# Optimization experiments

Measured on AMD Instinct MI355X. Metric: run time of the kernel, lower is better.

## Reference

```python
import jax, jax.numpy as jnp
import numpy as np

N = 50000   # nodes
E = 640000  # edges
IN = 256    # in_dim
H = 128     # hidden
OUT = 40    # out_dim
EPS = 1e-5  # BatchNorm eps


def setup_inputs() -> dict:
    key = jax.random.key(0)
    ks = jax.random.split(key, 14)
    x = jax.random.normal(ks[0], (N, IN), jnp.float32)
    edge_index = jax.random.randint(ks[1], (2, E), 0, N)
    def lin(k, fan_in, shape):
        return jax.random.normal(k, shape, jnp.float32) / np.float32(np.sqrt(fan_in))
    return {
        "x": x,
        "edge_index": edge_index,
        # block 0 (256 -> 128, has res_proj)
        "W0": lin(ks[2], IN, (IN, H)),
        "b0": jnp.zeros((H,), jnp.float32),
        "g0": jnp.ones((H,), jnp.float32),
        "be0": jnp.zeros((H,), jnp.float32),
        "pW": lin(ks[3], IN, (IN, H)),
        "pb": jnp.zeros((H,), jnp.float32),
        # block 1 (128 -> 128, identity residual)
        "W1": lin(ks[4], H, (H, H)),
        "b1": jnp.zeros((H,), jnp.float32),
        "g1": jnp.ones((H,), jnp.float32),
        "be1": jnp.zeros((H,), jnp.float32),
        # head
        "hW": lin(ks[5], H, (H, OUT)),
        "hb": jnp.zeros((OUT,), jnp.float32),
    }


def _gcn_conv(x, W, b, edge_index):
    """GCNConv(improved=True): x' = D^-1/2 (A + 2I) D^-1/2 (x W) + b."""
    h = x @ W  # [N, dout]
    row, col = edge_index[0], edge_index[1]  # source -> target
    # degree of A + 2I (edge_weight = 1, self-loop fill = 2.0)
    deg = jnp.zeros((N,), h.dtype).at[col].add(1.0) + 2.0
    dis = jax.lax.rsqrt(deg)  # deg > 0 always (self-loops)
    norm = dis[row] * dis[col]  # [E]
    # neighbor aggregation: scatter-add normalized messages to targets
    agg = jnp.zeros_like(h).at[col].add(norm[:, None] * h[row])
    # self-loop contribution with weight 2.0
    agg = agg + (2.0 * dis * dis)[:, None] * h
    return agg + b


def _bn(x, gamma, beta):
    # batch statistics (training-mode BatchNorm math), biased variance
    m = jnp.mean(x, axis=0)
    v = jnp.mean(jnp.square(x - m), axis=0)
    return (x - m) * jax.lax.rsqrt(v + EPS) * gamma + beta


def reference(x, edge_index, W0, b0, g0, be0, pW, pb, W1, b1, g1, be1, hW, hb):
    # block 0: conv -> bn -> relu -> (+ res_proj(x))
    out = jax.nn.relu(_bn(_gcn_conv(x, W0, b0, edge_index), g0, be0))
    x1 = out + (x @ pW + pb)
    # block 1: conv -> bn -> relu -> (+ identity)
    out = jax.nn.relu(_bn(_gcn_conv(x1, W1, b1, edge_index), g1, be1))
    x2 = out + x1
    return x2 @ hW + hb  # [N, OUT]
```

## Files before the change

kernel.cpp:

```cpp
#include <hip/hip_runtime.h>

#define H 128
#define IN_DIM 256
#define OUT_DIM 40
#define EPS 1e-5f

typedef unsigned short ushortT;
typedef __attribute__((ext_vector_type(8))) short bf16x8;
typedef __attribute__((ext_vector_type(4))) float f32x4;

static __device__ __forceinline__ ushortT f2bf(float f) {
    union { float f; unsigned u; } v; v.f = f;
    unsigned r = v.u + 0x7FFF + ((v.u >> 16) & 1);
    return (ushortT)(r >> 16);
}
static __device__ __forceinline__ unsigned pk2(float a, float b) {
    return (unsigned)f2bf(a) | ((unsigned)f2bf(b) << 16);
}
static __device__ __forceinline__ float bflo(unsigned v) {
    union { unsigned u; float f; } t; t.u = v << 16; return t.f;
}
static __device__ __forceinline__ float bfhi(unsigned v) {
    union { unsigned u; float f; } t; t.u = v & 0xFFFF0000u; return t.f;
}
static __device__ __forceinline__ float i2f(int v) {
    union { int i; float f; } t; t.i = v; return t.f;
}
static __device__ __forceinline__ int f2i(float v) {
    union { float f; int i; } t; t.f = v; return t.i;
}


__global__ __launch_bounds__(256) void count_xcd(const int* __restrict__ ei, int E, int nper,
                                                 int* __restrict__ cnt) {
    int xcd = blockIdx.x & 7;
    int nchunk = gridDim.x >> 3;
    int chunk = blockIdx.x >> 3;
    int csz = (E + nchunk - 1) / nchunk;
    int beg = chunk * csz;
    int end = min(E, beg + csz);
    for (int e = beg + (int)threadIdx.x; e < end; e += 256) {
        int c = ei[E + e];
        if (c / nper == xcd) atomicAdd(&cnt[c], 1);
    }
}

__global__ __launch_bounds__(256) void scan_block_sum(const int* __restrict__ cnt, int* __restrict__ bsum,
                                                      float* __restrict__ dis, int N) {
    __shared__ int s[256];
    int i = blockIdx.x * 256 + threadIdx.x;
    int c = (i < N) ? cnt[i] : -1;
    int v = (i < N) ? c + 1 : 0;
    if (i < N) dis[i] = rsqrtf((float)c + 2.0f);
    s[threadIdx.x] = v;
    __syncthreads();
    for (int o = 128; o > 0; o >>= 1) {
        if (threadIdx.x < o) s[threadIdx.x] += s[threadIdx.x + o];
        __syncthreads();
    }
    if (threadIdx.x == 0) bsum[blockIdx.x] = s[0];
}

__global__ void scan_tops(const int* __restrict__ bsum, int* __restrict__ boff, int* __restrict__ rowptrN, int nb) {
    __shared__ int s[256];
    int t = threadIdx.x;
    int v = (t < nb) ? bsum[t] : 0;
    s[t] = v;
    __syncthreads();
    for (int o = 1; o < 256; o <<= 1) {
        int u = (t >= o) ? s[t - o] : 0;
        __syncthreads();
        s[t] += u;
        __syncthreads();
    }
    if (t < nb) boff[t] = s[t] - v;
    if (t == 255) *rowptrN = s[255];
}

__global__ __launch_bounds__(256) void scan_final(const int* __restrict__ cnt, const int* __restrict__ boff,
                                                  const float* __restrict__ dis,
                                                  int* __restrict__ rowptr, int* __restrict__ cursor,
                                                  int2* __restrict__ recs, int N) {
    __shared__ int s[256];
    int t = threadIdx.x;
    int i = blockIdx.x * 256 + t;
    int v = (i < N) ? cnt[i] + 1 : 0;
    s[t] = v;
    __syncthreads();
    for (int o = 1; o < 256; o <<= 1) {
        int u = (t >= o) ? s[t - o] : 0;
        __syncthreads();
        s[t] += u;
        __syncthreads();
    }
    if (i < N) {
        int e = boff[blockIdx.x] + s[t] - v;
        rowptr[i] = e;
        cursor[i] = e + 1;
        float d = dis[i];
        int2 r; r.x = i; r.y = f2i(2.0f * d * d);
        recs[e] = r;
    }
}

__global__ __launch_bounds__(256) void fill_xcd(const int* __restrict__ ei, int E, int nper,
                                                const float* __restrict__ dis,
                                                int* __restrict__ cursor, int2* __restrict__ recs) {
    int xcd = blockIdx.x & 7;
    int nchunk = gridDim.x >> 3;
    int chunk = blockIdx.x >> 3;
    int csz = (E + nchunk - 1) / nchunk;
    int beg = chunk * csz;
    int end = min(E, beg + csz);
    for (int e = beg + (int)threadIdx.x; e < end; e += 256) {
        int c = ei[E + e];
        if (c / nper == xcd) {
            int r = ei[e];
            int slot = atomicAdd(&cursor[c], 1);
            int2 rec; rec.x = r; rec.y = f2i(dis[r] * dis[c]);
            recs[slot] = rec;
        }
    }
}


__global__ __launch_bounds__(256) void prep_weights(const float* __restrict__ W0, const float* __restrict__ pW,
                                                    const float* __restrict__ W1, const float* __restrict__ hW,
                                                    ushortT* __restrict__ Wt0, ushortT* __restrict__ WtP,
                                                    ushortT* __restrict__ Wt1, ushortT* __restrict__ WtH,
                                                    int* __restrict__ cnt, float* __restrict__ stats, int N) {
    int i = blockIdx.x * 256 + threadIdx.x;
    if (i < 32768) { int n = i >> 8, k = i & 255; Wt0[i] = f2bf(W0[k * 128 + n]); WtP[i] = f2bf(pW[k * 128 + n]); }
    if (i < 16384) { int n = i >> 7, k = i & 127; Wt1[i] = f2bf(W1[k * 128 + n]); }
    if (i < 6144)  { int n = i >> 7, k = i & 127; WtH[i] = (n < OUT_DIM) ? f2bf(hW[k * OUT_DIM + n]) : (ushortT)0; }
    if (i < N) cnt[i] = 0;
    if (i < 512) stats[i] = 0.f;
}


static __device__ __forceinline__ void g0_loads(const float* __restrict__ X, int brow, int kc,
                                                int tid, int N, float4 pf[4]) {
#pragma unroll
    for (int i = 0; i < 4; ++i) {
        int idx = i * 512 + tid;
        int row = idx >> 5, c4 = idx & 31;
        int gr = brow + row;
        pf[i] = make_float4(0.f, 0.f, 0.f, 0.f);
        if (gr < N) pf[i] = *(const float4*)&X[(size_t)gr * IN_DIM + kc * 128 + c4 * 4];
    }
}
static __device__ __forceinline__ void g0_write(ushortT* __restrict__ Sbuf, int tid, const float4 pf[4]) {
#pragma unroll
    for (int i = 0; i < 4; ++i) {
        int idx = i * 512 + tid;
        int row = idx >> 5, c4 = idx & 31;
        uint2 p;
        p.x = pk2(pf[i].x, pf[i].y);
        p.y = pk2(pf[i].z, pf[i].w);
        *(uint2*)&Sbuf[row * 136 + c4 * 4] = p;
    }
}

__global__ __launch_bounds__(512) void mgemm0p(const float* __restrict__ X,
                                               const ushortT* __restrict__ Wt0,
                                               const ushortT* __restrict__ WtP,
                                               const float* __restrict__ pb,
                                               ushortT* __restrict__ Oh,
                                               ushortT* __restrict__ Op,
                                               int N, int ntiles) {
    __shared__ __align__(16) ushortT S[2][64 * 136];
    int tid = threadIdx.x;
    int w = tid >> 6, lane = tid & 63;
    int lm = lane & 15, lk = lane >> 4;
    int mat = w >> 2;
    int colbase = (w & 3) * 32;
    const ushortT* Wt = mat ? WtP : Wt0;

    bf16x8 breg[2][8];
#pragma unroll
    for (int nt = 0; nt < 2; ++nt)
#pragma unroll
        for (int kk = 0; kk < 8; ++kk)
            breg[nt][kk] = *(const bf16x8*)&Wt[(size_t)(colbase + nt * 16 + lm) * IN_DIM + kk * 32 + lk * 8];
    float bb[2];
    bb[0] = mat ? pb[colbase + lm] : 0.f;
    bb[1] = mat ? pb[colbase + 16 + lm] : 0.f;
    ushortT* O = mat ? Op : Oh;

    int bid = blockIdx.x, G = gridDim.x;
    int T = (ntiles - 1 - bid) / G + 1;
    int U = 2 * T;

    float4 pf[4];
    g0_loads(X, bid * 64, 0, tid, N, pf);
    g0_write(S[0], tid, pf);

    f32x4 acc[4][2];
#pragma unroll
    for (int mt = 0; mt < 4; ++mt)
#pragma unroll
        for (int nt = 0; nt < 2; ++nt) acc[mt][nt] = (f32x4)0.f;

    for (int u = 0; u < U; ++u) {
        __syncthreads();
        if (u + 1 < U) {
            int t1 = bid + ((u + 1) >> 1) * G;
            g0_loads(X, t1 * 64, (u + 1) & 1, tid, N, pf);
        }
        int kc = u & 1;
        const ushortT* Sc = S[u & 1];
#pragma unroll
        for (int kk = 0; kk < 4; ++kk) {
            bf16x8 af[4];
#pragma unroll
            for (int mt = 0; mt < 4; ++mt)
                af[mt] = *(const bf16x8*)&Sc[(mt * 16 + lm) * 136 + kk * 32 + lk * 8];
#pragma unroll
            for (int nt = 0; nt < 2; ++nt)
#pragma unroll
                for (int mt = 0; mt < 4; ++mt)
                    acc[mt][nt] = __builtin_amdgcn_mfma_f32_16x16x32_bf16(af[mt], breg[nt][kc * 4 + kk], acc[mt][nt], 0, 0, 0);
        }
        if (u + 1 < U) g0_write(S[(u + 1) & 1], tid, pf);
        if (kc == 1) {
            int t = bid + (u >> 1) * G;
            int brow = t * 64;
#pragma unroll
            for (int mt = 0; mt < 4; ++mt)
#pragma unroll
                for (int nt = 0; nt < 2; ++nt) {
                    int col = colbase + nt * 16 + lm;
#pragma unroll
                    for (int j = 0; j < 4; ++j) {
                        int r = brow + mt * 16 + lk * 4 + j;
                        if (r < N) O[(size_t)r * 128 + col] = f2bf(acc[mt][nt][j] + bb[nt]);
                    }
                    acc[mt][nt] = (f32x4)0.f;
                }
        }
    }
}


__global__ __launch_bounds__(512) void mgemm1_fused(const uint4* __restrict__ aggb,
                                                    const uint4* __restrict__ projb,
                                                    const float* __restrict__ stats,
                                                    const float* __restrict__ g,
                                                    const float* __restrict__ be,
                                                    const ushortT* __restrict__ Wt1,
                                                    ushortT* __restrict__ O,
                                                    uint4* __restrict__ x1b,
                                                    int N) {
    __shared__ __align__(16) ushortT S[17408];
    __shared__ float sc[128], sh[128];
    int tid = threadIdx.x;
    int brow = blockIdx.x * 128;

    if (tid < 128) {
        float mean = stats[tid] / (float)N;
        float var = stats[128 + tid] / (float)N - mean * mean;
        float inv = rsqrtf(var + EPS);
        float s = g[tid] * inv;
        sc[tid] = s;
        sh[tid] = be[tid] - mean * s;
    }
    __syncthreads();

#pragma unroll
    for (int i = 0; i < 4; ++i) {
        int idx = i * 512 + tid;
        int row = idx >> 4, q = idx & 15;
        int gr = brow + row;
        uint4 a = make_uint4(0u, 0u, 0u, 0u), p = a;
        if (gr < N) {
            size_t gidx = (size_t)gr * 16 + q;
            a = aggb[gidx];
            p = projb[gidx];
        }
        int ch = q * 8;
        float v0 = fmaxf(fmaf(bflo(a.x), sc[ch + 0], sh[ch + 0]), 0.f) + bflo(p.x);
        float v1 = fmaxf(fmaf(bfhi(a.x), sc[ch + 1], sh[ch + 1]), 0.f) + bfhi(p.x);
        float v2 = fmaxf(fmaf(bflo(a.y), sc[ch + 2], sh[ch + 2]), 0.f) + bflo(p.y);
        float v3 = fmaxf(fmaf(bfhi(a.y), sc[ch + 3], sh[ch + 3]), 0.f) + bfhi(p.y);
        float v4 = fmaxf(fmaf(bflo(a.z), sc[ch + 4], sh[ch + 4]), 0.f) + bflo(p.z);
        float v5 = fmaxf(fmaf(bfhi(a.z), sc[ch + 5], sh[ch + 5]), 0.f) + bfhi(p.z);
        float v6 = fmaxf(fmaf(bflo(a.w), sc[ch + 6], sh[ch + 6]), 0.f) + bflo(p.w);
        float v7 = fmaxf(fmaf(bfhi(a.w), sc[ch + 7], sh[ch + 7]), 0.f) + bfhi(p.w);
        uint4 pv;
        pv.x = pk2(v0, v1);
        pv.y = pk2(v2, v3);
        pv.z = pk2(v4, v5);
        pv.w = pk2(v6, v7);
        *(uint4*)&S[row * 136 + q * 8] = pv;
        if (gr < N) x1b[(size_t)gr * 16 + q] = pv;
    }
    __syncthreads();

    int w = tid >> 6, lane = tid & 63;
    int lm = lane & 15, lk = lane >> 4;
    int rh = (w >> 2) * 64;
    int colbase = (w & 3) * 32;

    bf16x8 breg[2][4];
#pragma unroll
    for (int nt = 0; nt < 2; ++nt)
#pragma unroll
        for (int ks = 0; ks < 4; ++ks)
            breg[nt][ks] = *(const bf16x8*)&Wt1[(size_t)(colbase + nt * 16 + lm) * H + ks * 32 + lk * 8];

    f32x4 acc[4][2];
#pragma unroll
    for (int mt = 0; mt < 4; ++mt)
#pragma unroll
        for (int nt = 0; nt < 2; ++nt) acc[mt][nt] = (f32x4)0.f;

#pragma unroll
    for (int ks = 0; ks < 4; ++ks) {
        bf16x8 af[4];
#pragma unroll
        for (int mt = 0; mt < 4; ++mt)
            af[mt] = *(const bf16x8*)&S[(rh + mt * 16 + lm) * 136 + ks * 32 + lk * 8];
#pragma unroll
        for (int nt = 0; nt < 2; ++nt)
#pragma unroll
            for (int mt = 0; mt < 4; ++mt)
                acc[mt][nt] = __builtin_amdgcn_mfma_f32_16x16x32_bf16(af[mt], breg[nt][ks], acc[mt][nt], 0, 0, 0);
    }

    __syncthreads();
#pragma unroll
    for (int mt = 0; mt < 4; ++mt)
#pragma unroll
        for (int nt = 0; nt < 2; ++nt) {
            int col = colbase + nt * 16 + lm;
#pragma unroll
            for (int j = 0; j < 4; ++j) {
                int row = rh + mt * 16 + lk * 4 + j;
                S[row * 136 + col] = f2bf(acc[mt][nt][j]);
            }
        }
    __syncthreads();
#pragma unroll
    for (int i = 0; i < 4; ++i) {
        int idx = i * 512 + tid;
        int row = idx >> 4, colq = idx & 15;
        int gr = brow + row;
        if (gr < N) {
            uint4 v = *(const uint4*)&S[row * 136 + colq * 8];
            *(uint4*)&O[(size_t)gr * 128 + colq * 8] = v;
        }
    }
}


__global__ __launch_bounds__(256) void aggregate_rec(const ushortT* __restrict__ h,
                                                     const int* __restrict__ rowptr,
                                                     const int2* __restrict__ recs,
                                                     ushortT* __restrict__ aggb, int N) {
    int n = blockIdx.x * 4 + (threadIdx.x >> 6);
    if (n >= N) return;
    int lane = threadIdx.x & 63;
    int half = lane >> 5, cl = lane & 31;
    int beg = rowptr[n], end = rowptr[n + 1];
    const uint2* h2 = (const uint2*)h;
    float a0 = 0.f, a1 = 0.f, a2 = 0.f, a3 = 0.f;
    float b0 = 0.f, b1 = 0.f, b2 = 0.f, b3 = 0.f;
    int idx = beg + half;
    for (; idx + 2 < end; idx += 4) {
        int2 r0 = recs[idx];
        int2 r1 = recs[idx + 2];
        uint2 v0 = h2[(size_t)r0.x * 32 + cl];
        uint2 v1 = h2[(size_t)r1.x * 32 + cl];
        float n0 = i2f(r0.y), n1 = i2f(r1.y);
        a0 = fmaf(n0, bflo(v0.x), a0); a1 = fmaf(n0, bfhi(v0.x), a1);
        a2 = fmaf(n0, bflo(v0.y), a2); a3 = fmaf(n0, bfhi(v0.y), a3);
        b0 = fmaf(n1, bflo(v1.x), b0); b1 = fmaf(n1, bfhi(v1.x), b1);
        b2 = fmaf(n1, bflo(v1.y), b2); b3 = fmaf(n1, bfhi(v1.y), b3);
    }
    if (idx < end) {
        int2 r0 = recs[idx];
        uint2 v0 = h2[(size_t)r0.x * 32 + cl];
        float n0 = i2f(r0.y);
        a0 = fmaf(n0, bflo(v0.x), a0); a1 = fmaf(n0, bfhi(v0.x), a1);
        a2 = fmaf(n0, bflo(v0.y), a2); a3 = fmaf(n0, bfhi(v0.y), a3);
    }
    a0 += b0; a1 += b1; a2 += b2; a3 += b3;
    a0 += __shfl_xor(a0, 32);
    a1 += __shfl_xor(a1, 32);
    a2 += __shfl_xor(a2, 32);
    a3 += __shfl_xor(a3, 32);
    if (half == 0) {
        uint2 o;
        o.x = pk2(a0, a1);
        o.y = pk2(a2, a3);
        ((uint2*)aggb)[(size_t)n * 32 + cl] = o;
    }
}


__global__ __launch_bounds__(256) void stats_bf(const unsigned* __restrict__ v, int totalU,
                                                float* __restrict__ sums) {
    int tid = blockIdx.x * 256 + threadIdx.x;
    int stride = gridDim.x * 256;
    float sx = 0.f, sy = 0.f, qx = 0.f, qy = 0.f;
    for (int i = tid; i < totalU; i += stride) {
        unsigned u = v[i];
        float a = bflo(u), b = bfhi(u);
        sx += a; sy += b;
        qx = fmaf(a, a, qx); qy = fmaf(b, b, qy);
    }
    __shared__ float l0[256], l1[256], l2[256], l3[256];
    int t = threadIdx.x;
    l0[t] = sx; l1[t] = sy; l2[t] = qx; l3[t] = qy;
    __syncthreads();
    if (t < 64) {
        sx = (l0[t] + l0[t + 64]) + (l0[t + 128] + l0[t + 192]);
        sy = (l1[t] + l1[t + 64]) + (l1[t + 128] + l1[t + 192]);
        qx = (l2[t] + l2[t + 64]) + (l2[t + 128] + l2[t + 192]);
        qy = (l3[t] + l3[t + 64]) + (l3[t + 128] + l3[t + 192]);
        atomicAdd(&sums[2 * t], sx);
        atomicAdd(&sums[2 * t + 1], sy);
        atomicAdd(&sums[128 + 2 * t], qx);
        atomicAdd(&sums[128 + 2 * t + 1], qy);
    }
}


__global__ __launch_bounds__(256) void head_fused(const uint4* __restrict__ aggb,
                                                  const uint4* __restrict__ x1b,
                                                  const float* __restrict__ stats,
                                                  const float* __restrict__ g,
                                                  const float* __restrict__ be,
                                                  const ushortT* __restrict__ WtH,
                                                  const float* __restrict__ hb,
                                                  float* __restrict__ out, int N) {
    __shared__ __align__(16) ushortT As[64][136];
    __shared__ __align__(16) ushortT Bs[48][136];
    __shared__ float sc[128], sh[128];

    int tid = threadIdx.x;
    int brow = blockIdx.x * 64;
    int w = tid >> 6, lane = tid & 63;
    int lm = lane & 15, lk = lane >> 4;

    if (tid < 128) {
        float mean = stats[tid] / (float)N;
        float var = stats[128 + tid] / (float)N - mean * mean;
        float inv = rsqrtf(var + EPS);
        float s = g[tid] * inv;
        sc[tid] = s;
        sh[tid] = be[tid] - mean * s;
    }
    if (tid < 192) {
        int row = tid >> 2, q = tid & 3;
        const uint4* src = (const uint4*)&WtH[(size_t)row * H + q * 32];
        uint4 a = src[0], b = src[1], c = src[2], d = src[3];
        uint4* dst = (uint4*)&Bs[row][q * 32];
        dst[0] = a; dst[1] = b; dst[2] = c; dst[3] = d;
    }
    __syncthreads();
#pragma unroll
    for (int k = 0; k < 4; ++k) {
        int idx = k * 256 + tid;
        int row = idx >> 4, colq = idx & 15;
        int gr = brow + row;
        uint4 a = make_uint4(0u, 0u, 0u, 0u), x = a;
        if (gr < N) {
            size_t gidx = (size_t)brow * 16 + idx;
            a = aggb[gidx];
            x = x1b[gidx];
        }
        int ch = colq * 8;
        float v0 = fmaxf(fmaf(bflo(a.x), sc[ch + 0], sh[ch + 0]), 0.f) + bflo(x.x);
        float v1 = fmaxf(fmaf(bfhi(a.x), sc[ch + 1], sh[ch + 1]), 0.f) + bfhi(x.x);
        float v2 = fmaxf(fmaf(bflo(a.y), sc[ch + 2], sh[ch + 2]), 0.f) + bflo(x.y);
        float v3 = fmaxf(fmaf(bfhi(a.y), sc[ch + 3], sh[ch + 3]), 0.f) + bfhi(x.y);
        float v4 = fmaxf(fmaf(bflo(a.z), sc[ch + 4], sh[ch + 4]), 0.f) + bflo(x.z);
        float v5 = fmaxf(fmaf(bfhi(a.z), sc[ch + 5], sh[ch + 5]), 0.f) + bfhi(x.z);
        float v6 = fmaxf(fmaf(bflo(a.w), sc[ch + 6], sh[ch + 6]), 0.f) + bflo(x.w);
        float v7 = fmaxf(fmaf(bfhi(a.w), sc[ch + 7], sh[ch + 7]), 0.f) + bfhi(x.w);
        uint4 pv;
        pv.x = pk2(v0, v1);
        pv.y = pk2(v2, v3);
        pv.z = pk2(v4, v5);
        pv.w = pk2(v6, v7);
        *(uint4*)&As[row][colq * 8] = pv;
    }
    __syncthreads();

    f32x4 acc[3];
#pragma unroll
    for (int nt = 0; nt < 3; ++nt) acc[nt] = (f32x4)0.f;
#pragma unroll
    for (int ks = 0; ks < 4; ++ks) {
        bf16x8 a = *(const bf16x8*)&As[w * 16 + lm][ks * 32 + lk * 8];
#pragma unroll
        for (int nt = 0; nt < 3; ++nt) {
            bf16x8 b = *(const bf16x8*)&Bs[nt * 16 + lm][ks * 32 + lk * 8];
            acc[nt] = __builtin_amdgcn_mfma_f32_16x16x32_bf16(a, b, acc[nt], 0, 0, 0);
        }
    }
#pragma unroll
    for (int nt = 0; nt < 3; ++nt) {
        int col = nt * 16 + lm;
        if (col < OUT_DIM) {
            float bbv = hb[col];
#pragma unroll
            for (int j = 0; j < 4; ++j) {
                int r = brow + w * 16 + lk * 4 + j;
                if (r < N) out[(size_t)r * OUT_DIM + col] = acc[nt][j] + bbv;
            }
        }
    }
}


extern "C" void kernel_launch(void* const* d_in, const int* in_sizes, int n_in,
                              void* d_out, int out_size, void* d_ws, size_t ws_size,
                              hipStream_t stream) {
    const float* x   = (const float*)d_in[0];
    const int*   ei  = (const int*)d_in[1];
    const float* W0  = (const float*)d_in[2];
    const float* g0  = (const float*)d_in[4];
    const float* be0 = (const float*)d_in[5];
    const float* pW  = (const float*)d_in[6];
    const float* pb  = (const float*)d_in[7];
    const float* W1  = (const float*)d_in[8];
    const float* g1  = (const float*)d_in[10];
    const float* be1 = (const float*)d_in[11];
    const float* hW  = (const float*)d_in[12];
    const float* hb  = (const float*)d_in[13];
    float* out = (float*)d_out;

    int N = in_sizes[0] / IN_DIM;
    int E = in_sizes[1] / 2;
    size_t NH = (size_t)N * H;

    ushortT* hb16   = (ushortT*)d_ws;
    ushortT* aggb   = hb16 + NH;
    ushortT* projb  = aggb + NH;
    ushortT* x1b    = projb + NH;
    float*   dis    = (float*)(x1b + NH);
    int*     cnt    = (int*)(dis + N);
    int*     rowptr = cnt + N;
    int*     cursor = rowptr + (N + 1);
    int2*    recs   = (int2*)(cursor + N);
    float*   stats  = (float*)(recs + (E + N));
    ushortT* Wt0    = (ushortT*)(stats + 512);
    ushortT* WtP    = Wt0 + 128 * 256;
    ushortT* Wt1    = WtP + 128 * 256;
    ushortT* WtH    = Wt1 + 128 * 128;
    int*     bsum   = (int*)(WtH + 48 * 128);
    int*     boff   = bsum + 256;
    float*   stats0 = stats;
    float*   stats1 = stats + 256;

    int nb = (N + 255) / 256;
    int g64 = (N + 63) / 64;
    int g128 = (N + 127) / 128;
    int gAgg = (N + 3) / 4;
    int ntiles = g64;
    int gPersist = (ntiles + 1) / 2;

    prep_weights<<<196, 256, 0, stream>>>(W0, pW, W1, hW, Wt0, WtP, Wt1, WtH, cnt, stats, N);
    count_xcd<<<2048, 256, 0, stream>>>(ei, E, (N + 7) / 8, cnt);
    scan_block_sum<<<nb, 256, 0, stream>>>(cnt, bsum, dis, N);
    scan_tops<<<1, 256, 0, stream>>>(bsum, boff, &rowptr[N], nb);
    scan_final<<<nb, 256, 0, stream>>>(cnt, boff, dis, rowptr, cursor, recs, N);
    fill_xcd<<<2048, 256, 0, stream>>>(ei, E, (N + 7) / 8, dis, cursor, recs);

    mgemm0p<<<gPersist, 512, 0, stream>>>(x, Wt0, WtP, pb, hb16, projb, N, ntiles);
    aggregate_rec<<<gAgg, 256, 0, stream>>>(hb16, rowptr, recs, aggb, N);
    stats_bf<<<256, 256, 0, stream>>>((const unsigned*)aggb, (int)(NH / 2), stats0);

    mgemm1_fused<<<g128, 512, 0, stream>>>((const uint4*)aggb, (const uint4*)projb, stats0, g0, be0,
                                           Wt1, hb16, (uint4*)x1b, N);
    aggregate_rec<<<gAgg, 256, 0, stream>>>(hb16, rowptr, recs, aggb, N);
    stats_bf<<<256, 256, 0, stream>>>((const unsigned*)aggb, (int)(NH / 2), stats1);

    head_fused<<<g64, 256, 0, stream>>>((const uint4*)aggb, (const uint4*)x1b, stats1, g1, be1,
                                        WtH, hb, out, N);
}
```

Measured before the change: 261.6 us.

## Replace persistent first GEMM with one-tile-per-block kernel and staged coalesced stores

```diff
diff --git a/kernel.cpp b/kernel.cpp
--- a/kernel.cpp
+++ b/kernel.cpp
@@ -161,15 +161,16 @@
     }
 }
 
-__global__ __launch_bounds__(512) void mgemm0p(const float* __restrict__ X,
+__global__ __launch_bounds__(512) void mgemm0d(const float* __restrict__ X,
                                                const ushortT* __restrict__ Wt0,
                                                const ushortT* __restrict__ WtP,
                                                const float* __restrict__ pb,
                                                ushortT* __restrict__ Oh,
                                                ushortT* __restrict__ Op,
-                                               int N, int ntiles) {
-    __shared__ __align__(16) ushortT S[2][64 * 136];
+                                               int N) {
+    __shared__ __align__(16) ushortT S2[2][64 * 136];
     int tid = threadIdx.x;
+    int brow = blockIdx.x * 64;
     int w = tid >> 6, lane = tid & 63;
     int lm = lane & 15, lk = lane >> 4;
     int mat = w >> 2;
@@ -185,15 +186,12 @@
     float bb[2];
     bb[0] = mat ? pb[colbase + lm] : 0.f;
     bb[1] = mat ? pb[colbase + 16 + lm] : 0.f;
-    ushortT* O = mat ? Op : Oh;
-
-    int bid = blockIdx.x, G = gridDim.x;
-    int T = (ntiles - 1 - bid) / G + 1;
-    int U = 2 * T;
 
     float4 pf[4];
-    g0_loads(X, bid * 64, 0, tid, N, pf);
-    g0_write(S[0], tid, pf);
+    g0_loads(X, brow, 0, tid, N, pf);
+    g0_write(S2[0], tid, pf);
+    __syncthreads();
+    g0_loads(X, brow, 1, tid, N, pf);
 
     f32x4 acc[4][2];
 #pragma unroll
@@ -201,42 +199,56 @@
 #pragma unroll
         for (int nt = 0; nt < 2; ++nt) acc[mt][nt] = (f32x4)0.f;
 
-    for (int u = 0; u < U; ++u) {
-        __syncthreads();
-        if (u + 1 < U) {
-            int t1 = bid + ((u + 1) >> 1) * G;
-            g0_loads(X, t1 * 64, (u + 1) & 1, tid, N, pf);
-        }
-        int kc = u & 1;
-        const ushortT* Sc = S[u & 1];
-#pragma unroll
-        for (int kk = 0; kk < 4; ++kk) {
-            bf16x8 af[4];
+#pragma unroll
+    for (int kk = 0; kk < 4; ++kk) {
+        bf16x8 af[4];
+#pragma unroll
+        for (int mt = 0; mt < 4; ++mt)
+            af[mt] = *(const bf16x8*)&S2[0][(mt * 16 + lm) * 136 + kk * 32 + lk * 8];
+#pragma unroll
+        for (int nt = 0; nt < 2; ++nt)
 #pragma unroll
             for (int mt = 0; mt < 4; ++mt)
-                af[mt] = *(const bf16x8*)&Sc[(mt * 16 + lm) * 136 + kk * 32 + lk * 8];
-#pragma unroll
-            for (int nt = 0; nt < 2; ++nt)
-#pragma unroll
-                for (int mt = 0; mt < 4; ++mt)
-                    acc[mt][nt] = __builtin_amdgcn_mfma_f32_16x16x32_bf16(af[mt], breg[nt][kc * 4 + kk], acc[mt][nt], 0, 0, 0);
-        }
-        if (u + 1 < U) g0_write(S[(u + 1) & 1], tid, pf);
-        if (kc == 1) {
-            int t = bid + (u >> 1) * G;
-            int brow = t * 64;
+                acc[mt][nt] = __builtin_amdgcn_mfma_f32_16x16x32_bf16(af[mt], breg[nt][kk], acc[mt][nt], 0, 0, 0);
+    }
+    g0_write(S2[1], tid, pf);
+    __syncthreads();
+#pragma unroll
+    for (int kk = 0; kk < 4; ++kk) {
+        bf16x8 af[4];
+#pragma unroll
+        for (int mt = 0; mt < 4; ++mt)
+            af[mt] = *(const bf16x8*)&S2[1][(mt * 16 + lm) * 136 + kk * 32 + lk * 8];
+#pragma unroll
+        for (int nt = 0; nt < 2; ++nt)
 #pragma unroll
             for (int mt = 0; mt < 4; ++mt)
-#pragma unroll
-                for (int nt = 0; nt < 2; ++nt) {
-                    int col = colbase + nt * 16 + lm;
-#pragma unroll
-                    for (int j = 0; j < 4; ++j) {
-                        int r = brow + mt * 16 + lk * 4 + j;
-                        if (r < N) O[(size_t)r * 128 + col] = f2bf(acc[mt][nt][j] + bb[nt]);
-                    }
-                    acc[mt][nt] = (f32x4)0.f;
-                }
+                acc[mt][nt] = __builtin_amdgcn_mfma_f32_16x16x32_bf16(af[mt], breg[nt][4 + kk], acc[mt][nt], 0, 0, 0);
+    }
+    __syncthreads();
+#pragma unroll
+    for (int mt = 0; mt < 4; ++mt)
+#pragma unroll
+        for (int nt = 0; nt < 2; ++nt) {
+            int col = colbase + nt * 16 + lm;
+#pragma unroll
+            for (int j = 0; j < 4; ++j) {
+                int row = mt * 16 + lk * 4 + j;
+                S2[mat][row * 136 + col] = f2bf(acc[mt][nt][j] + bb[nt]);
+            }
+        }
+    __syncthreads();
+#pragma unroll
+    for (int i = 0; i < 4; ++i) {
+        int idx = i * 512 + tid;
+        int m2 = idx >> 10;
+        int rem = idx & 1023;
+        int row = rem >> 4, colq = rem & 15;
+        int gr = brow + row;
+        if (gr < N) {
+            uint4 v = *(const uint4*)&S2[m2][row * 136 + colq * 8];
+            ushortT* O = m2 ? Op : Oh;
+            *(uint4*)&O[(size_t)gr * 128 + colq * 8] = v;
         }
     }
 }
@@ -559,8 +571,6 @@
     int g64 = (N + 63) / 64;
     int g128 = (N + 127) / 128;
     int gAgg = (N + 3) / 4;
-    int ntiles = g64;
-    int gPersist = (ntiles + 1) / 2;
 
     prep_weights<<<196, 256, 0, stream>>>(W0, pW, W1, hW, Wt0, WtP, Wt1, WtH, cnt, stats, N);
     count_xcd<<<2048, 256, 0, stream>>>(ei, E, (N + 7) / 8, cnt);
@@ -569,7 +579,7 @@
     scan_final<<<nb, 256, 0, stream>>>(cnt, boff, dis, rowptr, cursor, recs, N);
     fill_xcd<<<2048, 256, 0, stream>>>(ei, E, (N + 7) / 8, dis, cursor, recs);
 
-    mgemm0p<<<gPersist, 512, 0, stream>>>(x, Wt0, WtP, pb, hb16, projb, N, ntiles);
+    mgemm0d<<<g64, 512, 0, stream>>>(x, Wt0, WtP, pb, hb16, projb, N);
     aggregate_rec<<<gAgg, 256, 0, stream>>>(hb16, rowptr, recs, aggb, N);
     stats_bf<<<256, 256, 0, stream>>>((const unsigned*)aggb, (int)(NH / 2), stats0);
 
```

Result: faster. 251.7 us (-3.8%).
